# Performance work log

Hardware: AMD Instinct MI355X
Metric: run time of the kernel (lower is better)

Reference implementation:

```python
import jax, jax.numpy as jnp
import numpy as np

B, J, T = 64, 24, 2048
FOOT_IDX = (7, 8, 10, 11)
LAMBDA_VEL = 0.2
LAMBDA_FOOT = 0.1
CONTACT_THRESH = 0.05


def setup_inputs() -> dict:
    key = jax.random.key(0)
    k1, k2, k3 = jax.random.split(key, 3)
    pred = jax.random.normal(k1, (B, J, 6, T), dtype=jnp.float32)
    target = jax.random.normal(k2, (B, J, 6, T), dtype=jnp.float32)
    joint_positions = jax.random.normal(k3, (B, J, 3, T), dtype=jnp.float32)
    return {"pred": pred, "target": target, "joint_positions": joint_positions}


def _foot_contact_loss(joint_positions):
    # joint_positions: [B, J, 3, T]
    foot_pos = joint_positions[:, jnp.array(FOOT_IDX), :, :]        # [B, F, 3, T]
    foot_height = foot_pos[:, :, 1, :]                              # [B, F, T]
    contact_w = jax.nn.sigmoid((CONTACT_THRESH - foot_height) * 20.0)
    foot_vel = foot_pos[:, :, :, 1:] - foot_pos[:, :, :, :-1]       # [B, F, 3, T-1]
    foot_vel_xz = foot_vel[:, :, jnp.array([0, 2]), :]              # [B, F, 2, T-1]
    cw_vel = (contact_w[:, :, 1:] + contact_w[:, :, :-1]) * 0.5     # [B, F, T-1]
    loss = (foot_vel_xz ** 2).sum(axis=2) * cw_vel                  # [B, F, T-1]
    num_contacts = cw_vel.sum() + 1e-8
    return loss.sum() / num_contacts


def reference(pred, target, joint_positions):
    # Reconstruction MSE on 6D rotations
    recon = jnp.mean((pred - target) ** 2)
    # First-order velocity loss over frames (last axis)
    dp = pred[:, :, :, 1:] - pred[:, :, :, :-1]
    dt = target[:, :, :, 1:] - target[:, :, :, :-1]
    vel = jnp.mean((dp - dt) ** 2)
    # Foot contact (anti-sliding) loss
    foot = _foot_contact_loss(joint_positions)
    total = recon + LAMBDA_VEL * vel + LAMBDA_FOOT * foot
    return total
```

## Files before the change

kernel.cpp:

```cpp
#include <hip/hip_runtime.h>

#define BB 64
#define JJ 24
#define TT 2048
#define NELEM (BB*JJ*6*TT)
#define NVEL  ((long long)BB*JJ*6*(TT-1))
#define FOOT_BLOCKS 256
#define RBLOCKS 4608
#define NRT (RBLOCKS*256)
#define NBLK (FOOT_BLOCKS + RBLOCKS)

__device__ __forceinline__ void block_reduce2f(float& a, float& b) {
    #pragma unroll
    for (int off = 32; off > 0; off >>= 1) {
        a += __shfl_down(a, off);
        b += __shfl_down(b, off);
    }
    __shared__ float sa[4], sb[4];
    const int lane = threadIdx.x & 63;
    const int wid  = threadIdx.x >> 6;
    if (lane == 0) { sa[wid] = a; sb[wid] = b; }
    __syncthreads();
    if (threadIdx.x == 0) {
        for (int w = 1; w < 4; ++w) { a += sa[w]; b += sb[w]; }
    }
}

__device__ __forceinline__ float sigm(float y) {
    return 1.f / (1.f + __expf(-(0.05f - y) * 20.f));
}

__global__ __launch_bounds__(256) void fused_kernel(
        const float* __restrict__ pred, const float* __restrict__ targ,
        const float* __restrict__ jp, double2* __restrict__ parts) {

    if (blockIdx.x < FOOT_BLOCKS) {
        const int FI[4] = {7, 8, 10, 11};
        const int bf = blockIdx.x;
        const int b  = bf >> 2;
        const int j  = FI[bf & 3];
        const float* __restrict__ xrow = jp + ((size_t)(b * JJ + j) * 3) * TT;
        const float* __restrict__ yrow = xrow + TT;
        const float* __restrict__ zrow = xrow + 2 * TT;
        const float4* __restrict__ x4 = reinterpret_cast<const float4*>(xrow);
        const float4* __restrict__ y4 = reinterpret_cast<const float4*>(yrow);
        const float4* __restrict__ z4 = reinterpret_cast<const float4*>(zrow);

        float lsum = 0.f, csum = 0.f;
        #pragma unroll
        for (int cc = 0; cc < 2; ++cc) {
            const int c = threadIdx.x + cc * 256;
            const float4 xv = x4[c], yv = y4[c], zv = z4[c];
            float x0 = 0.f, y0 = 0.f, z0 = 0.f;
            if (c > 0) { x0 = xrow[4*c-1]; y0 = yrow[4*c-1]; z0 = zrow[4*c-1]; }
            const float w0 = sigm(y0),  w1 = sigm(yv.x), w2 = sigm(yv.y),
                        w3 = sigm(yv.z), w4 = sigm(yv.w);
            auto term = [&](float x1, float xp, float z1, float zp,
                            float wa, float wb) {
                const float cw = 0.5f * (wa + wb);
                const float vx = x1 - xp, vz = z1 - zp;
                lsum += (vx * vx + vz * vz) * cw;
                csum += cw;
            };
            if (c > 0) term(xv.x, x0, zv.x, z0, w1, w0);
            term(xv.y, xv.x, zv.y, zv.x, w2, w1);
            term(xv.z, xv.y, zv.z, zv.y, w3, w2);
            term(xv.w, xv.z, zv.w, zv.z, w4, w3);
        }
        block_reduce2f(lsum, csum);
        if (threadIdx.x == 0)
            parts[blockIdx.x] = make_double2((double)lsum, (double)csum);
    } else {
        const int tid = (blockIdx.x - FOOT_BLOCKS) * 256 + threadIdx.x;
        const float4* __restrict__ pred4 = reinterpret_cast<const float4*>(pred);
        const float4* __restrict__ targ4 = reinterpret_cast<const float4*>(targ);
        const bool hasb = (tid & 511) != 0;

        float4 P[4], G[4];
        float pm[4], gm[4];
        #pragma unroll
        for (int k = 0; k < 4; ++k) {
            const int c = tid + k * NRT;
            P[k] = pred4[c];
            G[k] = targ4[c];
        }
        #pragma unroll
        for (int k = 0; k < 4; ++k) {
            const int e = 4 * (tid + k * NRT);
            pm[k] = hasb ? pred[e - 1] : 0.f;
            gm[k] = hasb ? targ[e - 1] : 0.f;
        }

        float recon = 0.f, vel = 0.f;
        #pragma unroll
        for (int k = 0; k < 4; ++k) {
            const float d0 = P[k].x - G[k].x, d1 = P[k].y - G[k].y,
                        d2 = P[k].z - G[k].z, d3 = P[k].w - G[k].w;
            recon += d0*d0 + d1*d1 + d2*d2 + d3*d3;
            const float e01 = d1 - d0, e12 = d2 - d1, e23 = d3 - d2;
            vel += e01*e01 + e12*e12 + e23*e23;
            if (hasb) { const float b0 = d0 - (pm[k] - gm[k]); vel += b0 * b0; }
        }

        block_reduce2f(recon, vel);
        if (threadIdx.x == 0)
            parts[blockIdx.x] = make_double2((double)recon, (double)vel);
    }
}

__global__ __launch_bounds__(256) void finalize_kernel(
        const double2* __restrict__ parts, float* __restrict__ out) {
    double fl = 0.0, fc = 0.0, rc = 0.0, vl = 0.0;
    for (int i = threadIdx.x; i < NBLK; i += 256) {
        const double2 v = parts[i];
        if (i < FOOT_BLOCKS) { fl += v.x; fc += v.y; }
        else                 { rc += v.x; vl += v.y; }
    }
    #pragma unroll
    for (int off = 32; off > 0; off >>= 1) {
        rc += __shfl_down(rc, off);
        vl += __shfl_down(vl, off);
        fl += __shfl_down(fl, off);
        fc += __shfl_down(fc, off);
    }
    __shared__ double s4[4][4];
    const int lane = threadIdx.x & 63, wid = threadIdx.x >> 6;
    if (lane == 0) { s4[wid][0]=rc; s4[wid][1]=vl; s4[wid][2]=fl; s4[wid][3]=fc; }
    __syncthreads();
    if (threadIdx.x == 0) {
        for (int w = 1; w < 4; ++w) {
            rc += s4[w][0]; vl += s4[w][1]; fl += s4[w][2]; fc += s4[w][3];
        }
        const double r = rc / (double)NELEM;
        const double v = vl / (double)NVEL;
        const double f = fl / (fc + 1e-8);
        out[0] = (float)(r + 0.2 * v + 0.1 * f);
    }
}

extern "C" void kernel_launch(void* const* d_in, const int* in_sizes, int n_in,
                              void* d_out, int out_size, void* d_ws, size_t ws_size,
                              hipStream_t stream) {
    const float* pred = (const float*)d_in[0];
    const float* targ = (const float*)d_in[1];
    const float* jp   = (const float*)d_in[2];
    float* out     = (float*)d_out;
    double2* parts = (double2*)d_ws;

    fused_kernel<<<NBLK, 256, 0, stream>>>(pred, targ, jp, parts);
    finalize_kernel<<<1, 256, 0, stream>>>(parts, out);
}
```

Measured before the change: 190.1 us.

## Use grid-stride loop with prefetch and shuffle neighbor exchange for recon/vel

The recon/velocity path now uses fewer blocks, each thread looping over nine float4 chunks with a software-prefetched next iteration. The previous element for the velocity boundary now comes from the neighbouring lane via __shfl_up instead of an extra scalar global load, so only wave-leading lanes do that scalar load. This cuts redundant misaligned loads and per-block reduction overhead. In exchange it adds a serial loop dependency and has less memory-level parallelism per thread than the previous four-way unrolled loads.

```diff
diff --git a/kernel.cpp b/kernel.cpp
--- a/kernel.cpp
+++ b/kernel.cpp
@@ -6,9 +6,11 @@
 #define NELEM (BB*JJ*6*TT)
 #define NVEL  ((long long)BB*JJ*6*(TT-1))
 #define FOOT_BLOCKS 256
-#define RBLOCKS 4608
-#define NRT (RBLOCKS*256)
-#define NBLK (FOOT_BLOCKS + RBLOCKS)
+#define RGRID 2048
+#define NTH (RGRID*256)
+#define NC4 (NELEM/4)
+#define ITERS 9
+#define NBLK (FOOT_BLOCKS + RGRID)
 
 __device__ __forceinline__ void block_reduce2f(float& a, float& b) {
     #pragma unroll
@@ -71,35 +73,39 @@
         if (threadIdx.x == 0)
             parts[blockIdx.x] = make_double2((double)lsum, (double)csum);
     } else {
-        const int tid = (blockIdx.x - FOOT_BLOCKS) * 256 + threadIdx.x;
+        const int t = (blockIdx.x - FOOT_BLOCKS) * 256 + threadIdx.x;
         const float4* __restrict__ pred4 = reinterpret_cast<const float4*>(pred);
         const float4* __restrict__ targ4 = reinterpret_cast<const float4*>(targ);
-        const bool hasb = (tid & 511) != 0;
+        const bool hasb  = (t & 511) != 0;
+        const bool lead  = (threadIdx.x & 63) == 0;
 
-        float4 P[4], G[4];
-        float pm[4], gm[4];
-        #pragma unroll
-        for (int k = 0; k < 4; ++k) {
-            const int c = tid + k * NRT;
-            P[k] = pred4[c];
-            G[k] = targ4[c];
-        }
-        #pragma unroll
-        for (int k = 0; k < 4; ++k) {
-            const int e = 4 * (tid + k * NRT);
-            pm[k] = hasb ? pred[e - 1] : 0.f;
-            gm[k] = hasb ? targ[e - 1] : 0.f;
-        }
+        float4 P0 = pred4[t], G0 = targ4[t];
+        float pmg0 = 0.f;
+        if (lead && hasb) pmg0 = pred[4*t - 1] - targ[4*t - 1];
 
         float recon = 0.f, vel = 0.f;
-        #pragma unroll
-        for (int k = 0; k < 4; ++k) {
-            const float d0 = P[k].x - G[k].x, d1 = P[k].y - G[k].y,
-                        d2 = P[k].z - G[k].z, d3 = P[k].w - G[k].w;
+        #pragma unroll 1
+        for (int k = 0; k < ITERS; ++k) {
+            float4 P1, G1;
+            float pmg1 = 0.f;
+            if (k + 1 < ITERS) {
+                const int c = t + (k + 1) * NTH;
+                P1 = pred4[c];
+                G1 = targ4[c];
+                if (lead && hasb) pmg1 = pred[4*c - 1] - targ[4*c - 1];
+            }
+
+            const float d0 = P0.x - G0.x, d1 = P0.y - G0.y,
+                        d2 = P0.z - G0.z, d3 = P0.w - G0.w;
             recon += d0*d0 + d1*d1 + d2*d2 + d3*d3;
             const float e01 = d1 - d0, e12 = d2 - d1, e23 = d3 - d2;
             vel += e01*e01 + e12*e12 + e23*e23;
-            if (hasb) { const float b0 = d0 - (pm[k] - gm[k]); vel += b0 * b0; }
+
+            float prev = __shfl_up(d3, 1);
+            if (lead) prev = pmg0;
+            if (hasb) { const float b0 = d0 - prev; vel += b0 * b0; }
+
+            P0 = P1; G0 = G1; pmg0 = pmg1;
         }
 
         block_reduce2f(recon, vel);
```

Measured after the change: 189.3 us. No clear change (-0.4%).
